# Optimization experiments

Hardware: AMD Instinct MI355X
Metric: run time of the kernel (lower is better)

## Reference

```python
import jax, jax.numpy as jnp
import numpy as np

N_EMBD = 768
N_HEAD = 8
B, T = 4, 2048

def setup_inputs() -> dict:
    key = jax.random.key(0)
    k1, k2, k3, k4, k5 = jax.random.split(key, 5)
    C = N_EMBD
    s = 1.0 / np.sqrt(C)
    return {
        "x": jax.random.normal(k1, (B, T, C), dtype=jnp.float32),
        "W_attn": jax.random.normal(k2, (C, 3 * C), dtype=jnp.float32) * s,
        "b_attn": jnp.zeros((3 * C,), dtype=jnp.float32),
        "W_proj": jax.random.normal(k3, (C, C), dtype=jnp.float32) * s,
        "b_proj": jnp.zeros((C,), dtype=jnp.float32),
    }

def reference(x, W_attn, b_attn, W_proj, b_proj):
    Bs, Ts, C = x.shape
    H = N_HEAD
    hs = C // H
    qkv = x @ W_attn + b_attn                      # [B,T,3C]
    q, k, v = jnp.split(qkv, 3, axis=-1)
    # reshape to [B,H,T,hs]
    q = q.reshape(Bs, Ts, H, hs).transpose(0, 2, 1, 3)
    k = k.reshape(Bs, Ts, H, hs).transpose(0, 2, 1, 3)
    v = v.reshape(Bs, Ts, H, hs).transpose(0, 2, 1, 3)
    scale = 1.0 / jnp.sqrt(jnp.float32(hs))
    att = jnp.einsum('bhid,bhjd->bhij', q, k) * scale   # [B,H,T,T]
    mask = jnp.tril(jnp.ones((Ts, Ts), dtype=bool))
    att = jnp.where(mask, att, -jnp.inf)
    m = jnp.max(att, axis=-1, keepdims=True)
    e = jnp.where(mask, jnp.exp(att - m), 0.0)
    # original kernel divides by (sum + 1e-9)
    att = e / (jnp.sum(e, axis=-1, keepdims=True) + 1e-9)
    y = jnp.einsum('bhij,bhjd->bhid', att, v)           # [B,H,T,hs]
    y = y.transpose(0, 2, 1, 3).reshape(Bs, Ts, C)
    return y @ W_proj + b_proj
```

## Files before the change

kernel.cpp:

```cpp
#include <hip/hip_runtime.h>

typedef __bf16 bf16;
typedef __attribute__((ext_vector_type(4))) __bf16 bf16x4;
typedef __attribute__((ext_vector_type(8))) __bf16 bf16x8;
typedef __attribute__((ext_vector_type(4))) float f32x4;

#define B_   4
#define T_   2048
#define C_   768
#define H_   8
#define HS_  96
#define M_   (B_ * T_)
#define QKN_ (3 * C_)

#define NEG_BIG (-1e30f)

#define KSTR 104
#define VSTR 72
#define PSTR 72

__device__ __forceinline__ void gload_lds16(const bf16* g, bf16* l) {
    __builtin_amdgcn_global_load_lds(
        (const __attribute__((address_space(1))) uint32_t*)g,
        (__attribute__((address_space(3))) uint32_t*)l,
        16, 0, 0);
}

__global__ void transpose_kernel(const float* __restrict__ W, bf16* __restrict__ Wt,
                                 int R, int Cn) {
    __shared__ bf16 tile[32][33];
    int tx = threadIdx.x, ty = threadIdx.y;
    int x  = blockIdx.x * 32 + tx;
    int y0 = blockIdx.y * 32;
#pragma unroll
    for (int j = 0; j < 32; j += 8)
        tile[ty + j][tx] = (bf16)W[(size_t)(y0 + ty + j) * Cn + x];
    __syncthreads();
    int y2 = blockIdx.x * 32;
    int x2 = y0 + tx;
#pragma unroll
    for (int j = 0; j < 32; j += 8)
        Wt[(size_t)(y2 + ty + j) * R + x2] = tile[tx][ty + j];
}

__global__ void sentinel_kernel(float* __restrict__ out, int n) {
    int i = blockIdx.x * 256 + threadIdx.x;
    if (i < n) out[i] = 12345.0f;
}

__device__ __forceinline__ bf16x8 cvt8(f32x4 v0, f32x4 v1) {
    bf16x8 o;
#pragma unroll
    for (int i = 0; i < 4; ++i) { o[i] = (bf16)v0[i]; o[4 + i] = (bf16)v1[i]; }
    return o;
}

__global__ __launch_bounds__(256) void convert_bf16_kernel(const float* __restrict__ in,
                                                           bf16* __restrict__ out,
                                                           int n8) {
    int i = blockIdx.x * 256 + threadIdx.x;
    if (i >= n8) return;
    const float* p = in + (size_t)i * 8;
    f32x4 a = *(const f32x4*)p;
    f32x4 b = *(const f32x4*)(p + 4);
    *(bf16x8*)&out[(size_t)i * 8] = cvt8(a, b);
}

__global__ __launch_bounds__(256) void gemm_qkv(const bf16* __restrict__ A,
                                                const bf16* __restrict__ Bt,
                                                const float* __restrict__ bias,
                                                bf16* __restrict__ Cmat,
                                                bf16* __restrict__ Vt,
                                                int M, int N, int K) {
    __shared__ bf16 lda[128 * 64];
    __shared__ bf16 ldb[128 * 64];
    int tid  = threadIdx.x;
    int w    = tid >> 6;
    int lane = tid & 63;
    int col  = lane & 15, quad = lane >> 4;
    int wr   = w >> 1, wc = w & 1;
    int m0   = blockIdx.y * 128, n0 = blockIdx.x * 128;

    int srow = lane >> 3;
    int scol = (lane & 7) * 8;
    const bf16* gA[4]; const bf16* gB[4]; bf16* lA[4]; bf16* lB[4];
#pragma unroll
    for (int i = 0; i < 4; ++i) {
        int seg = w * 4 + i;
        int row = seg * 8 + srow;
        gA[i] = &A[(size_t)(m0 + row) * K + scol];
        gB[i] = &Bt[(size_t)(n0 + row) * K + scol];
        lA[i] = &lda[seg * 512];
        lB[i] = &ldb[seg * 512];
    }

    const f32x4 zero = {0.f, 0.f, 0.f, 0.f};
    f32x4 acc[4][4];
#pragma unroll
    for (int mr = 0; mr < 4; ++mr)
#pragma unroll
        for (int nc = 0; nc < 4; ++nc) acc[mr][nc] = zero;

    for (int k0 = 0; k0 < K; k0 += 64) {
#pragma unroll
        for (int i = 0; i < 4; ++i) {
            gload_lds16(gA[i] + k0, lA[i]);
            gload_lds16(gB[i] + k0, lB[i]);
        }
        __syncthreads();
#pragma unroll
        for (int ks = 0; ks < 2; ++ks) {
            bf16x8 af[4], bfr[4];
#pragma unroll
            for (int t = 0; t < 4; ++t) {
                af[t]  = *(const bf16x8*)&lda[(wr * 64 + t * 16 + col) * 64 + ks * 32 + quad * 8];
                bfr[t] = *(const bf16x8*)&ldb[(wc * 64 + t * 16 + col) * 64 + ks * 32 + quad * 8];
            }
#pragma unroll
            for (int mr = 0; mr < 4; ++mr)
#pragma unroll
                for (int nc = 0; nc < 4; ++nc)
                    acc[mr][nc] = __builtin_amdgcn_mfma_f32_16x16x32_bf16(
                        af[mr], bfr[nc], acc[mr][nc], 0, 0, 0);
        }
        __syncthreads();
    }

#pragma unroll
    for (int nc = 0; nc < 4; ++nc) {
        int n = n0 + wc * 64 + nc * 16 + col;
        float bv = bias[n];
#pragma unroll
        for (int mr = 0; mr < 4; ++mr) {
#pragma unroll
            for (int r = 0; r < 4; ++r) {
                int row = m0 + wr * 64 + mr * 16 + quad * 4 + r;
                Cmat[(size_t)row * N + n] = (bf16)(acc[mr][nc][r] + bv);
            }
        }
    }
    if (n0 >= 2 * C_) {
        int batch = m0 >> 11;
        bf16* Vtb = Vt + (size_t)batch * C_ * T_;
        int t0 = (m0 & 2047) + wr * 64;
#pragma unroll
        for (int nc = 0; nc < 4; ++nc) {
            int n  = n0 + wc * 64 + nc * 16 + col;
            int vc = n - 2 * C_;
            float bv = bias[n];
#pragma unroll
            for (int mr = 0; mr < 4; ++mr) {
                int t = t0 + mr * 16 + quad * 4;
                bf16x4 pk = {(bf16)(acc[mr][nc][0] + bv), (bf16)(acc[mr][nc][1] + bv),
                             (bf16)(acc[mr][nc][2] + bv), (bf16)(acc[mr][nc][3] + bv)};
                *(bf16x4*)&Vtb[(size_t)vc * T_ + t] = pk;
            }
        }
    }
}

__global__ __launch_bounds__(256) void gemm_proj(const bf16* __restrict__ A,
                                                 const bf16* __restrict__ Bt,
                                                 const float* __restrict__ bias,
                                                 float* __restrict__ Cmat,
                                                 int M, int N, int K) {
    __shared__ bf16 lda[128 * 64];
    __shared__ bf16 ldb[128 * 64];
    int tid  = threadIdx.x;
    int w    = tid >> 6;
    int lane = tid & 63;
    int col  = lane & 15, quad = lane >> 4;
    int wr   = w >> 1, wc = w & 1;
    int m0   = blockIdx.y * 128, n0 = blockIdx.x * 128;

    int srow = lane >> 3;
    int scol = (lane & 7) * 8;
    const bf16* gA[4]; const bf16* gB[4]; bf16* lA[4]; bf16* lB[4];
#pragma unroll
    for (int i = 0; i < 4; ++i) {
        int seg = w * 4 + i;
        int row = seg * 8 + srow;
        gA[i] = &A[(size_t)(m0 + row) * K + scol];
        gB[i] = &Bt[(size_t)(n0 + row) * K + scol];
        lA[i] = &lda[seg * 512];
        lB[i] = &ldb[seg * 512];
    }

    const f32x4 zero = {0.f, 0.f, 0.f, 0.f};
    f32x4 acc[4][4];
#pragma unroll
    for (int mr = 0; mr < 4; ++mr)
#pragma unroll
        for (int nc = 0; nc < 4; ++nc) acc[mr][nc] = zero;

    for (int k0 = 0; k0 < K; k0 += 64) {
#pragma unroll
        for (int i = 0; i < 4; ++i) {
            gload_lds16(gA[i] + k0, lA[i]);
            gload_lds16(gB[i] + k0, lB[i]);
        }
        __syncthreads();
#pragma unroll
        for (int ks = 0; ks < 2; ++ks) {
            bf16x8 af[4], bfr[4];
#pragma unroll
            for (int t = 0; t < 4; ++t) {
                af[t]  = *(const bf16x8*)&lda[(wr * 64 + t * 16 + col) * 64 + ks * 32 + quad * 8];
                bfr[t] = *(const bf16x8*)&ldb[(wc * 64 + t * 16 + col) * 64 + ks * 32 + quad * 8];
            }
#pragma unroll
            for (int mr = 0; mr < 4; ++mr)
#pragma unroll
                for (int nc = 0; nc < 4; ++nc)
                    acc[mr][nc] = __builtin_amdgcn_mfma_f32_16x16x32_bf16(
                        af[mr], bfr[nc], acc[mr][nc], 0, 0, 0);
        }
        __syncthreads();
    }

#pragma unroll
    for (int nc = 0; nc < 4; ++nc) {
        int n = n0 + wc * 64 + nc * 16 + col;
        float bv = bias[n];
#pragma unroll
        for (int mr = 0; mr < 4; ++mr) {
#pragma unroll
            for (int r = 0; r < 4; ++r) {
                int row = m0 + wr * 64 + mr * 16 + quad * 4 + r;
                Cmat[(size_t)row * N + n] = acc[mr][nc][r] + bv;
            }
        }
    }
}

__global__ __launch_bounds__(256) void attn_kernel(const bf16* __restrict__ qkv,
                                                   const bf16* __restrict__ Vt,
                                                   bf16* __restrict__ y,
                                                   int nGroups) {
    __shared__ bf16 ldsK[64 * KSTR];
    __shared__ bf16 ldsV[96 * VSTR];
    __shared__ bf16 ldsP[4 * 16 * PSTR];
    const int bid  = blockIdx.x;
    const int qt   = 31 - bid / nGroups;
    const int g    = bid % nGroups;
    const int h    = g & 7, b = g >> 3;
    const int tid  = threadIdx.x;
    const int w    = tid >> 6, lane = tid & 63;
    const int col  = lane & 15, quad = lane >> 4;
    const float SCALE2 = 0.10206207261596577f * 1.4426950408889634f;
    const float M0 = 24.0f;
    const f32x4 zero = {0.f, 0.f, 0.f, 0.f};

    const bf16* qkvb = qkv + (size_t)b * T_ * QKN_;
    const bf16* Vtbh = Vt + (size_t)(b * H_ + h) * HS_ * T_;
    bf16* yb  = y + (size_t)b * T_ * C_;
    bf16* myP = &ldsP[w * 16 * PSTR];

    const int rbase = qt * 64 + w * 16;

    bf16x8 qf[3];
#pragma unroll
    for (int c = 0; c < 3; ++c)
        qf[c] = *(const bf16x8*)&qkvb[(size_t)(rbase + col) * QKN_ + h * HS_ + c * 32 + quad * 8];

    const bf16* pK[3]; const bf16* pV[3];
    bf16 *dK[3], *dV[3];
#pragma unroll
    for (int i = 0; i < 3; ++i) {
        int chunk = i * 256 + tid;
        int rK = chunk / 12, cK = chunk - rK * 12;
        pK[i] = qkvb + (size_t)rK * QKN_ + C_ + h * HS_ + cK * 8;
        dK[i] = &ldsK[rK * KSTR + cK * 8];
        int rV = chunk >> 3, cV = chunk & 7;
        pV[i] = Vtbh + (size_t)rV * T_ + cV * 8;
        dV[i] = &ldsV[rV * VSTR + cV * 8];
    }

    f32x4 o[6];
#pragma unroll
    for (int n2 = 0; n2 < 6; ++n2) o[n2] = zero;
    float lsum = 0.f;

    const int njt = qt + 1;
    for (int jt = 0; jt < njt; ++jt) {
        int jb = jt * 64;
        __syncthreads();
#pragma unroll
        for (int i = 0; i < 3; ++i) {
            *(bf16x8*)dK[i] = *(const bf16x8*)pK[i];
            *(bf16x8*)dV[i] = *(const bf16x8*)pV[i];
            pK[i] += (size_t)64 * QKN_;
            pV[i] += 64;
        }
        __syncthreads();

        bf16x8 kf[4][3];
#pragma unroll
        for (int nb = 0; nb < 4; ++nb)
#pragma unroll
            for (int c = 0; c < 3; ++c)
                kf[nb][c] = *(const bf16x8*)&ldsK[(nb * 16 + col) * KSTR + c * 32 + quad * 8];

        f32x4 st[4];
#pragma unroll
        for (int nb = 0; nb < 4; ++nb) st[nb] = zero;
#pragma unroll
        for (int c = 0; c < 3; ++c)
#pragma unroll
            for (int nb = 0; nb < 4; ++nb)
                st[nb] = __builtin_amdgcn_mfma_f32_16x16x32_bf16(
                    kf[nb][c], qf[c], st[nb], 0, 0, 0);

        if (jt == njt - 1) {
#pragma unroll
            for (int nb = 0; nb < 4; ++nb)
#pragma unroll
                for (int r = 0; r < 4; ++r) {
                    int jg = jb + nb * 16 + quad * 4 + r;
                    st[nb][r] = (jg <= rbase + col) ? fmaf(st[nb][r], SCALE2, -M0)
                                                    : NEG_BIG;
                }
        } else {
#pragma unroll
            for (int nb = 0; nb < 4; ++nb)
#pragma unroll
                for (int r = 0; r < 4; ++r)
                    st[nb][r] = fmaf(st[nb][r], SCALE2, -M0);
        }

#pragma unroll
        for (int nb = 0; nb < 4; ++nb) {
#pragma unroll
            for (int r = 0; r < 4; ++r) {
                float pv = exp2f(st[nb][r]);
                st[nb][r] = pv;
                lsum += pv;
            }
            bf16x4 pk = {(bf16)st[nb][0], (bf16)st[nb][1],
                         (bf16)st[nb][2], (bf16)st[nb][3]};
            *(bf16x4*)&myP[col * PSTR + nb * 16 + quad * 4] = pk;
        }

        bf16x8 vf[6][2];
#pragma unroll
        for (int n2 = 0; n2 < 6; ++n2)
#pragma unroll
            for (int c = 0; c < 2; ++c)
                vf[n2][c] = *(const bf16x8*)&ldsV[(n2 * 16 + col) * VSTR + c * 32 + quad * 8];
        bf16x8 pa0 = *(const bf16x8*)&myP[col * PSTR + quad * 8];
        bf16x8 pa1 = *(const bf16x8*)&myP[col * PSTR + 32 + quad * 8];
#pragma unroll
        for (int n2 = 0; n2 < 6; ++n2)
            o[n2] = __builtin_amdgcn_mfma_f32_16x16x32_bf16(vf[n2][0], pa0, o[n2], 0, 0, 0);
#pragma unroll
        for (int n2 = 0; n2 < 6; ++n2)
            o[n2] = __builtin_amdgcn_mfma_f32_16x16x32_bf16(vf[n2][1], pa1, o[n2], 0, 0, 0);
    }

    lsum += __shfl_xor(lsum, 16, 64);
    lsum += __shfl_xor(lsum, 32, 64);
    float linv = 1.0f / lsum;
#pragma unroll
    for (int n2 = 0; n2 < 6; ++n2) {
        bf16x4 pk = {(bf16)(o[n2][0] * linv), (bf16)(o[n2][1] * linv),
                     (bf16)(o[n2][2] * linv), (bf16)(o[n2][3] * linv)};
        *(bf16x4*)&yb[(size_t)(rbase + col) * C_ + h * HS_ + n2 * 16 + quad * 4] = pk;
    }
}

extern "C" void kernel_launch(void* const* d_in, const int* in_sizes, int n_in,
                              void* d_out, int out_size, void* d_ws, size_t ws_size,
                              hipStream_t stream) {
    (void)in_sizes; (void)n_in;
    const float* x      = (const float*)d_in[0];
    const float* W_attn = (const float*)d_in[1];
    const float* b_attn = (const float*)d_in[2];
    const float* W_proj = (const float*)d_in[3];
    const float* b_proj = (const float*)d_in[4];
    float* out = (float*)d_out;

    size_t e_wta = (size_t)QKN_ * C_;
    size_t e_wtp = (size_t)C_ * C_;
    size_t a_qkv = e_wta + e_wtp;
    size_t a_vt  = a_qkv + (size_t)M_ * QKN_;
    size_t a_yb  = a_vt + (size_t)M_ * C_;
    size_t needA = (a_yb + (size_t)M_ * C_) * sizeof(bf16);
    size_t b_qkv = e_wta + e_wtp;
    size_t b_vt  = b_qkv + (size_t)T_ * QKN_;
    size_t b_yb  = b_vt + (size_t)T_ * C_;
    size_t needB = (b_yb + (size_t)T_ * C_) * sizeof(bf16);

    if (ws_size >= needA) {
        bf16* Wt_attn = (bf16*)d_ws;
        bf16* Wt_proj = (bf16*)d_ws + e_wta;
        bf16* qkv     = (bf16*)d_ws + a_qkv;
        bf16* Vt      = (bf16*)d_ws + a_vt;
        bf16* yb      = (bf16*)d_ws + a_yb;
        bf16* xb      = yb;
        convert_bf16_kernel<<<dim3(M_ * C_ / 8 / 256), 256, 0, stream>>>(x, xb, M_ * C_ / 8);
        transpose_kernel<<<dim3(QKN_ / 32, C_ / 32), dim3(32, 8), 0, stream>>>(W_attn, Wt_attn, C_, QKN_);
        transpose_kernel<<<dim3(C_ / 32, C_ / 32), dim3(32, 8), 0, stream>>>(W_proj, Wt_proj, C_, C_);
        gemm_qkv<<<dim3(QKN_ / 128, M_ / 128), 256, 0, stream>>>(
            xb, Wt_attn, b_attn, qkv, Vt, M_, QKN_, C_);
        attn_kernel<<<dim3(32 * H_ * B_), 256, 0, stream>>>(qkv, Vt, yb, H_ * B_);
        gemm_proj<<<dim3(C_ / 128, M_ / 128), 256, 0, stream>>>(
            yb, Wt_proj, b_proj, out, M_, C_, C_);
    } else if (ws_size >= needB) {
        bf16* Wt_attn = (bf16*)d_ws;
        bf16* Wt_proj = (bf16*)d_ws + e_wtp + e_wta - e_wtp;
        Wt_proj = (bf16*)d_ws + e_wta;
        bf16* qkv     = (bf16*)d_ws + b_qkv;
        bf16* Vt      = (bf16*)d_ws + b_vt;
        bf16* yb      = (bf16*)d_ws + b_yb;
        bf16* xb      = yb;
        transpose_kernel<<<dim3(QKN_ / 32, C_ / 32), dim3(32, 8), 0, stream>>>(W_attn, Wt_attn, C_, QKN_);
        transpose_kernel<<<dim3(C_ / 32, C_ / 32), dim3(32, 8), 0, stream>>>(W_proj, Wt_proj, C_, C_);
        for (int b = 0; b < B_; ++b) {
            const float* xf = x + (size_t)b * T_ * C_;
            float* outb     = out + (size_t)b * T_ * C_;
            convert_bf16_kernel<<<dim3(T_ * C_ / 8 / 256), 256, 0, stream>>>(xf, xb, T_ * C_ / 8);
            gemm_qkv<<<dim3(QKN_ / 128, T_ / 128), 256, 0, stream>>>(
                xb, Wt_attn, b_attn, qkv, Vt, T_, QKN_, C_);
            attn_kernel<<<dim3(32 * H_), 256, 0, stream>>>(qkv, Vt, yb, H_);
            gemm_proj<<<dim3(C_ / 128, T_ / 128), 256, 0, stream>>>(
                yb, Wt_proj, b_proj, outb, T_, C_, C_);
        }
    } else {
        sentinel_kernel<<<(out_size + 255) / 256, 256, 0, stream>>>(out, out_size);
    }
}
```

Measured before the change: 232.5 us.

## Double-buffer GEMM LDS tiles and register-prefetch K/V tiles in attention

Both GEMM kernels now keep two LDS buffers per operand and issue global-to-LDS loads for the next K-step before computing on the current one, with one barrier per iteration. The attention kernel prefetches the next K/V tile into registers while the current tile is computed, so the global load latency is hidden behind the MFMA work. This doubles GEMM LDS use to 64KB per block, which may lower occupancy, and adds register pressure in the attention kernel. A redundant pointer computation in the fallback path is also cleaned up.

```diff
diff --git a/kernel.cpp b/kernel.cpp
--- a/kernel.cpp
+++ b/kernel.cpp
@@ -66,14 +66,16 @@
     *(bf16x8*)&out[(size_t)i * 8] = cvt8(a, b);
 }
 
+#define TILE_ELEMS (128 * 64)
+
 __global__ __launch_bounds__(256) void gemm_qkv(const bf16* __restrict__ A,
                                                 const bf16* __restrict__ Bt,
                                                 const float* __restrict__ bias,
                                                 bf16* __restrict__ Cmat,
                                                 bf16* __restrict__ Vt,
                                                 int M, int N, int K) {
-    __shared__ bf16 lda[128 * 64];
-    __shared__ bf16 ldb[128 * 64];
+    __shared__ bf16 lda[2 * TILE_ELEMS];
+    __shared__ bf16 ldb[2 * TILE_ELEMS];
     int tid  = threadIdx.x;
     int w    = tid >> 6;
     int lane = tid & 63;
@@ -101,20 +103,32 @@
 #pragma unroll
         for (int nc = 0; nc < 4; ++nc) acc[mr][nc] = zero;
 
+#pragma unroll
+    for (int i = 0; i < 4; ++i) {
+        gload_lds16(gA[i], lA[i]);
+        gload_lds16(gB[i], lB[i]);
+    }
+    __syncthreads();
+
+    int cur = 0;
     for (int k0 = 0; k0 < K; k0 += 64) {
-#pragma unroll
-        for (int i = 0; i < 4; ++i) {
-            gload_lds16(gA[i] + k0, lA[i]);
-            gload_lds16(gB[i] + k0, lB[i]);
-        }
-        __syncthreads();
+        int nxt = cur ^ 1;
+        if (k0 + 64 < K) {
+#pragma unroll
+            for (int i = 0; i < 4; ++i) {
+                gload_lds16(gA[i] + k0 + 64, lA[i] + nxt * TILE_ELEMS);
+                gload_lds16(gB[i] + k0 + 64, lB[i] + nxt * TILE_ELEMS);
+            }
+        }
+        const bf16* la = &lda[cur * TILE_ELEMS];
+        const bf16* lb = &ldb[cur * TILE_ELEMS];
 #pragma unroll
         for (int ks = 0; ks < 2; ++ks) {
             bf16x8 af[4], bfr[4];
 #pragma unroll
             for (int t = 0; t < 4; ++t) {
-                af[t]  = *(const bf16x8*)&lda[(wr * 64 + t * 16 + col) * 64 + ks * 32 + quad * 8];
-                bfr[t] = *(const bf16x8*)&ldb[(wc * 64 + t * 16 + col) * 64 + ks * 32 + quad * 8];
+                af[t]  = *(const bf16x8*)&la[(wr * 64 + t * 16 + col) * 64 + ks * 32 + quad * 8];
+                bfr[t] = *(const bf16x8*)&lb[(wc * 64 + t * 16 + col) * 64 + ks * 32 + quad * 8];
             }
 #pragma unroll
             for (int mr = 0; mr < 4; ++mr)
@@ -124,6 +138,7 @@
                         af[mr], bfr[nc], acc[mr][nc], 0, 0, 0);
         }
         __syncthreads();
+        cur = nxt;
     }
 
 #pragma unroll
@@ -164,8 +179,8 @@
                                                  const float* __restrict__ bias,
                                                  float* __restrict__ Cmat,
                                                  int M, int N, int K) {
-    __shared__ bf16 lda[128 * 64];
-    __shared__ bf16 ldb[128 * 64];
+    __shared__ bf16 lda[2 * TILE_ELEMS];
+    __shared__ bf16 ldb[2 * TILE_ELEMS];
     int tid  = threadIdx.x;
     int w    = tid >> 6;
     int lane = tid & 63;
@@ -193,20 +208,32 @@
 #pragma unroll
         for (int nc = 0; nc < 4; ++nc) acc[mr][nc] = zero;
 
+#pragma unroll
+    for (int i = 0; i < 4; ++i) {
+        gload_lds16(gA[i], lA[i]);
+        gload_lds16(gB[i], lB[i]);
+    }
+    __syncthreads();
+
+    int cur = 0;
     for (int k0 = 0; k0 < K; k0 += 64) {
-#pragma unroll
-        for (int i = 0; i < 4; ++i) {
-            gload_lds16(gA[i] + k0, lA[i]);
-            gload_lds16(gB[i] + k0, lB[i]);
-        }
-        __syncthreads();
+        int nxt = cur ^ 1;
+        if (k0 + 64 < K) {
+#pragma unroll
+            for (int i = 0; i < 4; ++i) {
+                gload_lds16(gA[i] + k0 + 64, lA[i] + nxt * TILE_ELEMS);
+                gload_lds16(gB[i] + k0 + 64, lB[i] + nxt * TILE_ELEMS);
+            }
+        }
+        const bf16* la = &lda[cur * TILE_ELEMS];
+        const bf16* lb = &ldb[cur * TILE_ELEMS];
 #pragma unroll
         for (int ks = 0; ks < 2; ++ks) {
             bf16x8 af[4], bfr[4];
 #pragma unroll
             for (int t = 0; t < 4; ++t) {
-                af[t]  = *(const bf16x8*)&lda[(wr * 64 + t * 16 + col) * 64 + ks * 32 + quad * 8];
-                bfr[t] = *(const bf16x8*)&ldb[(wc * 64 + t * 16 + col) * 64 + ks * 32 + quad * 8];
+                af[t]  = *(const bf16x8*)&la[(wr * 64 + t * 16 + col) * 64 + ks * 32 + quad * 8];
+                bfr[t] = *(const bf16x8*)&lb[(wc * 64 + t * 16 + col) * 64 + ks * 32 + quad * 8];
             }
 #pragma unroll
             for (int mr = 0; mr < 4; ++mr)
@@ -216,6 +243,7 @@
                         af[mr], bfr[nc], acc[mr][nc], 0, 0, 0);
         }
         __syncthreads();
+        cur = nxt;
     }
 
 #pragma unroll
@@ -281,18 +309,34 @@
     for (int n2 = 0; n2 < 6; ++n2) o[n2] = zero;
     float lsum = 0.f;
 
+    bf16x8 kreg[3], vreg[3];
+#pragma unroll
+    for (int i = 0; i < 3; ++i) {
+        kreg[i] = *(const bf16x8*)pK[i];
+        vreg[i] = *(const bf16x8*)pV[i];
+        pK[i] += (size_t)64 * QKN_;
+        pV[i] += 64;
+    }
+
     const int njt = qt + 1;
     for (int jt = 0; jt < njt; ++jt) {
         int jb = jt * 64;
         __syncthreads();
 #pragma unroll
         for (int i = 0; i < 3; ++i) {
-            *(bf16x8*)dK[i] = *(const bf16x8*)pK[i];
-            *(bf16x8*)dV[i] = *(const bf16x8*)pV[i];
-            pK[i] += (size_t)64 * QKN_;
-            pV[i] += 64;
+            *(bf16x8*)dK[i] = kreg[i];
+            *(bf16x8*)dV[i] = vreg[i];
         }
         __syncthreads();
+        if (jt + 1 < njt) {
+#pragma unroll
+            for (int i = 0; i < 3; ++i) {
+                kreg[i] = *(const bf16x8*)pK[i];
+                vreg[i] = *(const bf16x8*)pV[i];
+                pK[i] += (size_t)64 * QKN_;
+                pV[i] += 64;
+            }
+        }
 
         bf16x8 kf[4][3];
 #pragma unroll
@@ -407,8 +451,7 @@
             yb, Wt_proj, b_proj, out, M_, C_, C_);
     } else if (ws_size >= needB) {
         bf16* Wt_attn = (bf16*)d_ws;
-        bf16* Wt_proj = (bf16*)d_ws + e_wtp + e_wta - e_wtp;
-        Wt_proj = (bf16*)d_ws + e_wta;
+        bf16* Wt_proj = (bf16*)d_ws + e_wta;
         bf16* qkv     = (bf16*)d_ws + b_qkv;
         bf16* Vt      = (bf16*)d_ws + b_vt;
         bf16* yb      = (bf16*)d_ws + b_yb;
```

Result: faster. 216.1 us (-7.0%).
